# Optimization experiments

Hardware: AMD Instinct MI355X
Metric: run time of the kernel (lower is better)

## Reference

```python
import jax, jax.numpy as jnp
import numpy as np

CHANNELS = 512
NUM_HEADS = 8
GROUPS = 32
EPS = 1e-5  # torch GroupNorm default


def setup_inputs() -> dict:
    key = jax.random.key(0)
    ks = jax.random.split(key, 7)
    B, C, H, W = 16, CHANNELS, 64, 64
    x = jax.random.normal(ks[0], (B, C, H, W), dtype=jnp.float32)
    # GroupNorm affine params (torch init: weight=1, bias=0; randomize slightly for a nontrivial baseline)
    gamma = jnp.ones((C,), jnp.float32) + 0.02 * jax.random.normal(ks[1], (C,), jnp.float32)
    beta = 0.02 * jax.random.normal(ks[2], (C,), jnp.float32)
    # 1x1 convs == dense matrices over channel dim
    w_qkv = jax.random.normal(ks[3], (3 * C, C), jnp.float32) / np.sqrt(C)
    b_qkv = 0.01 * jax.random.normal(ks[4], (3 * C,), jnp.float32)
    w_proj = jax.random.normal(ks[5], (C, C), jnp.float32) / np.sqrt(C)
    b_proj = 0.01 * jax.random.normal(ks[6], (C,), jnp.float32)
    return {"x": x, "gamma": gamma, "beta": beta, "w_qkv": w_qkv,
            "b_qkv": b_qkv, "w_proj": w_proj, "b_proj": b_proj}


def _group_norm(x, gamma, beta):
    B, C, H, W = x.shape
    xg = x.reshape(B, GROUPS, C // GROUPS, H, W)
    mean = jnp.mean(xg, axis=(2, 3, 4), keepdims=True)
    var = jnp.mean(jnp.square(xg - mean), axis=(2, 3, 4), keepdims=True)
    xn = ((xg - mean) * jax.lax.rsqrt(var + EPS)).reshape(B, C, H, W)
    return xn * gamma[:, None, None] + beta[:, None, None]


def reference(x, gamma, beta, w_qkv, b_qkv, w_proj, b_proj):
    B, C, H, W = x.shape
    h = NUM_HEADS
    d = C // h  # head_dim
    residual = x
    xn = _group_norm(x, gamma, beta)
    # 1x1 conv == per-pixel dense layer over channels
    qkv = jnp.einsum('bchw,oc->bohw', xn, w_qkv) + b_qkv[:, None, None]
    q, k, v = jnp.split(qkv, 3, axis=1)
    N = H * W
    # rearrange 'b (h c) h1 w1 -> b h c (h1 w1)': rows = head_dim, cols = spatial
    q = q.reshape(B, h, d, N)
    k = k.reshape(B, h, d, N)
    v = v.reshape(B, h, d, N)
    scale = d ** (-0.5)
    # attention over head_dim axis (faithful to the source rearrange)
    attn = jax.nn.softmax(jnp.einsum('bhcn,bhdn->bhcd', q, k) * scale, axis=-1)  # [B,h,d,d]
    out = jnp.einsum('bhcd,bhdn->bhcn', attn, v).reshape(B, C, H, W)
    out = jnp.einsum('bchw,oc->bohw', out, w_proj) + b_proj[:, None, None]
    return out + residual
```

## Files before the change

kernel.cpp:

```cpp
#include <hip/hip_runtime.h>

typedef unsigned short u16;
typedef __attribute__((ext_vector_type(8))) short short8;
typedef __attribute__((ext_vector_type(4))) float floatx4;
typedef __attribute__((ext_vector_type(4))) unsigned int uintx4;

#define B_    16
#define C_    512
#define N_    4096
#define NH_   8
#define HD_   64
#define MQKV  1536

union V16 { uintx4 u; u16 s[8]; short8 h; };

__device__ inline u16 f2bf(float f) {
  union { float f; unsigned int i; } c; c.f = f;
  unsigned int i = c.i;
  return (u16)((i + 0x7FFFu + ((i >> 16) & 1u)) >> 16);
}

__device__ __forceinline__ void gld16(const u16* g, u16* l) {
  __builtin_amdgcn_global_load_lds(
      (const __attribute__((address_space(1))) unsigned int*)g,
      (__attribute__((address_space(3))) unsigned int*)l, 16, 0, 0);
}

__global__ __launch_bounds__(256) void gn_stats(const float* __restrict__ x,
    const float* __restrict__ gamma, const float* __restrict__ beta,
    float* __restrict__ s_arr, float* __restrict__ t_arr) {
  int b = blockIdx.x >> 5, g = blockIdx.x & 31;
  const floatx4* p = (const floatx4*)(x + (size_t)(b * C_ + g * 16) * N_);
  int tid = threadIdx.x;
  float sum = 0.f, ssq = 0.f;
  for (int it = 0; it < 64; ++it) {
    floatx4 v = p[tid + it * 256];
#pragma unroll
    for (int j = 0; j < 4; ++j) { float f = v[j]; sum += f; ssq += f * f; }
  }
#pragma unroll
  for (int off = 32; off > 0; off >>= 1) {
    sum += __shfl_down(sum, off);
    ssq += __shfl_down(ssq, off);
  }
  __shared__ float red[8];
  __shared__ float mv[2];
  int lane = tid & 63, wid = tid >> 6;
  if (lane == 0) { red[wid] = sum; red[wid + 4] = ssq; }
  __syncthreads();
  if (tid == 0) {
    float s = red[0] + red[1] + red[2] + red[3];
    float q = red[4] + red[5] + red[6] + red[7];
    float mean = s * (1.f / 65536.f);
    float var  = q * (1.f / 65536.f) - mean * mean;
    mv[0] = mean; mv[1] = rsqrtf(var + 1e-5f);
  }
  __syncthreads();
  if (tid < 16) {
    int c = g * 16 + tid;
    float ga = gamma[c], be = beta[c];
    float mean = mv[0], rstd = mv[1];
    s_arr[b * C_ + c] = ga * rstd;
    t_arr[b * C_ + c] = be - mean * rstd * ga;
  }
}

__global__ __launch_bounds__(256) void cvt_bf16(const float* __restrict__ src,
                                                u16* __restrict__ dst) {
  int i = blockIdx.x * 256 + threadIdx.x;
  const floatx4* s4 = (const floatx4*)src;
  floatx4 a = s4[2 * i], b = s4[2 * i + 1];
  V16 v;
#pragma unroll
  for (int j = 0; j < 4; ++j) { v.s[j] = f2bf(a[j]); v.s[4 + j] = f2bf(b[j]); }
  ((uintx4*)dst)[i] = v.u;
}

__global__ __launch_bounds__(256) void gn_apply_t(const float* __restrict__ x,
    const float* __restrict__ s_arr, const float* __restrict__ t_arr,
    u16* __restrict__ xt, int b0) {
  __shared__ float T[64][65];
  int bz = blockIdx.z, gb = b0 + bz;
  int n0 = blockIdx.x * 64, c0 = blockIdx.y * 64;
  int tid = threadIdx.x;
  int cl = tid >> 4;
  int nl = (tid & 15) * 4;
  const float* xb = x + (size_t)bz * C_ * N_;
#pragma unroll
  for (int ci = 0; ci < 4; ++ci) {
    int c = c0 + cl + ci * 16;
    float s = s_arr[gb * C_ + c], t = t_arr[gb * C_ + c];
    floatx4 v = *(const floatx4*)(xb + (size_t)c * N_ + n0 + nl);
#pragma unroll
    for (int j = 0; j < 4; ++j) T[cl + ci * 16][nl + j] = s * v[j] + t;
  }
  __syncthreads();
  int n = tid >> 2, cc = (tid & 3) * 16;
  V16 a, b;
#pragma unroll
  for (int j = 0; j < 8; ++j) a.s[j] = f2bf(T[cc + j][n]);
#pragma unroll
  for (int j = 0; j < 8; ++j) b.s[j] = f2bf(T[cc + 8 + j][n]);
  uintx4* dst = (uintx4*)(xt + (size_t)bz * N_ * C_ + (size_t)(n0 + n) * C_ + c0 + cc);
  dst[0] = a.u; dst[1] = b.u;
}

__global__ __launch_bounds__(256) void gemm_bt(
    const u16* __restrict__ A, const u16* __restrict__ Bm,
    const float* __restrict__ bias, const float* __restrict__ resid,
    void* __restrict__ outv, int M, int doRes, int outF32) {
  __shared__ alignas(16) u16 As[128 * 64];
  __shared__ alignas(16) u16 Bs[128 * 64];
  int bz = blockIdx.z;
  int m0 = blockIdx.y * 128, n0 = blockIdx.x * 128;
  int tid = threadIdx.x, lane = tid & 63, wid = tid >> 6;
  int quad = lane >> 4, l15 = lane & 15;
  int wm = (wid >> 1) * 64, wn = (wid & 1) * 64;
  int sr = tid >> 3, sc = tid & 7;
  const u16* Bb = Bm + (size_t)bz * ((size_t)N_ * C_);
  floatx4 acc[4][4];
#pragma unroll
  for (int i = 0; i < 4; ++i)
#pragma unroll
    for (int j = 0; j < 4; ++j) acc[i][j] = (floatx4)0.f;

  for (int kt = 0; kt < 8; ++kt) {
#pragma unroll
    for (int i = 0; i < 4; ++i) {
      int rr = sr + i * 32;
      int cc = sc ^ (rr & 7);
      gld16(A  + (size_t)(m0 + rr) * C_ + kt * 64 + cc * 8, &As[rr * 64 + sc * 8]);
      gld16(Bb + (size_t)(n0 + rr) * C_ + kt * 64 + cc * 8, &Bs[rr * 64 + sc * 8]);
    }
    __syncthreads();
#pragma unroll
    for (int ks = 0; ks < 2; ++ks) {
      short8 af[4], bf8[4];
#pragma unroll
      for (int mi = 0; mi < 4; ++mi) {
        int row = wm + mi * 16 + l15;
        int kc = (ks * 4 + quad) ^ (row & 7);
        af[mi] = *(const short8*)&As[row * 64 + kc * 8];
      }
#pragma unroll
      for (int ni = 0; ni < 4; ++ni) {
        int row = wn + ni * 16 + l15;
        int kc = (ks * 4 + quad) ^ (row & 7);
        bf8[ni] = *(const short8*)&Bs[row * 64 + kc * 8];
      }
#pragma unroll
      for (int mi = 0; mi < 4; ++mi)
#pragma unroll
        for (int ni = 0; ni < 4; ++ni)
          acc[mi][ni] = __builtin_amdgcn_mfma_f32_16x16x32_bf16(af[mi], bf8[ni], acc[mi][ni], 0, 0, 0);
    }
    __syncthreads();
  }
#pragma unroll
  for (int mi = 0; mi < 4; ++mi) {
#pragma unroll
    for (int ni = 0; ni < 4; ++ni) {
#pragma unroll
      for (int r = 0; r < 4; ++r) {
        int o = m0 + wm + mi * 16 + quad * 4 + r;
        int n = n0 + wn + ni * 16 + l15;
        float vv = acc[mi][ni][r] + bias[o];
        size_t oidx = ((size_t)bz * M + o) * N_ + n;
        if (doRes) vv += resid[oidx];
        if (outF32) ((float*)outv)[oidx] = vv;
        else        ((u16*)outv)[oidx]   = f2bf(vv);
      }
    }
  }
}

__global__ __launch_bounds__(256) void qk_softmax(const u16* __restrict__ qkv,
                                                  float* __restrict__ attn) {
  int h = blockIdx.x, bz = blockIdx.y;
  const u16* qb = qkv + ((size_t)bz * MQKV + h * HD_) * N_;
  const u16* kb = qkv + ((size_t)bz * MQKV + C_ + h * HD_) * N_;
  int tid = threadIdx.x, lane = tid & 63, wid = tid >> 6;
  int quad = lane >> 4, l15 = lane & 15;
  floatx4 acc[4][4];
#pragma unroll
  for (int i = 0; i < 4; ++i)
#pragma unroll
    for (int j = 0; j < 4; ++j) acc[i][j] = (floatx4)0.f;

  for (int ks = 0; ks < 32; ++ks) {
    int n = wid * 1024 + ks * 32 + quad * 8;
    short8 af[4], bf8[4];
#pragma unroll
    for (int mi = 0; mi < 4; ++mi)
      af[mi] = *(const short8*)(qb + (size_t)(mi * 16 + l15) * N_ + n);
#pragma unroll
    for (int ni = 0; ni < 4; ++ni)
      bf8[ni] = *(const short8*)(kb + (size_t)(ni * 16 + l15) * N_ + n);
#pragma unroll
    for (int mi = 0; mi < 4; ++mi)
#pragma unroll
      for (int ni = 0; ni < 4; ++ni)
        acc[mi][ni] = __builtin_amdgcn_mfma_f32_16x16x32_bf16(af[mi], bf8[ni], acc[mi][ni], 0, 0, 0);
  }
  __shared__ float S[64 * 65];
  for (int i = tid; i < 64 * 65; i += 256) S[i] = 0.f;
  __syncthreads();
#pragma unroll
  for (int mi = 0; mi < 4; ++mi)
#pragma unroll
    for (int ni = 0; ni < 4; ++ni)
#pragma unroll
      for (int r = 0; r < 4; ++r)
        atomicAdd(&S[(mi * 16 + quad * 4 + r) * 65 + ni * 16 + l15], acc[mi][ni][r]);
  __syncthreads();
  if (tid < 64) {
    float mx = -1e30f;
    for (int j = 0; j < 64; ++j) mx = fmaxf(mx, S[tid * 65 + j]);
    float sum = 0.f;
    for (int j = 0; j < 64; ++j) sum += __expf((S[tid * 65 + j] - mx) * 0.125f);
    float inv = 1.f / sum;
    float* dst = attn + ((size_t)(bz * NH_ + h) * 64 + tid) * 64;
    for (int j = 0; j < 64; ++j) dst[j] = __expf((S[tid * 65 + j] - mx) * 0.125f) * inv;
  }
}

__global__ __launch_bounds__(256) void pv_kernel(const float* __restrict__ attn,
    const u16* __restrict__ qkv, u16* __restrict__ ot) {
  int nt = blockIdx.x, h = blockIdx.y, bz = blockIdx.z;
  int n0 = nt * 256;
  const u16* vb = qkv + ((size_t)bz * MQKV + 2 * C_ + h * HD_) * N_;
  __shared__ alignas(16) u16 Ps[64 * 72];
  __shared__ alignas(16) u16 Vs[256 * 72];
  int tid = threadIdx.x, lane = tid & 63, wid = tid >> 6;
  int quad = lane >> 4, l15 = lane & 15;
  const float* ab = attn + (size_t)(bz * NH_ + h) * 4096;
#pragma unroll
  for (int i = 0; i < 16; ++i) {
    int idx = tid + i * 256;
    int row = idx >> 6, col = idx & 63;
    Ps[row * 72 + col] = f2bf(ab[idx]);
  }
#pragma unroll
  for (int i = 0; i < 8; ++i) {
    int l = tid + i * 256;
    int ch = l >> 5, n8 = (l & 31) * 8;
    V16 v; v.u = *(const uintx4*)(vb + (size_t)ch * N_ + n0 + n8);
    int chunk = ch >> 3, clo = ch & 7;
#pragma unroll
    for (int j = 0; j < 8; ++j) {
      int nl = n8 + j;
      Vs[nl * 72 + (chunk ^ ((nl >> 3) & 7)) * 8 + clo] = v.s[j];
    }
  }
  __syncthreads();
  floatx4 acc[4][4];
#pragma unroll
  for (int i = 0; i < 4; ++i)
#pragma unroll
    for (int j = 0; j < 4; ++j) acc[i][j] = (floatx4)0.f;
#pragma unroll
  for (int ks = 0; ks < 2; ++ks) {
    short8 af[4], bf8[4];
    int ko = ks * 32 + quad * 8;
#pragma unroll
    for (int mi = 0; mi < 4; ++mi)
      af[mi] = *(const short8*)&Ps[(mi * 16 + l15) * 72 + ko];
    int chunk = ks * 4 + quad;
#pragma unroll
    for (int ni = 0; ni < 4; ++ni) {
      int nl = wid * 64 + ni * 16 + l15;
      bf8[ni] = *(const short8*)&Vs[nl * 72 + (chunk ^ ((nl >> 3) & 7)) * 8];
    }
#pragma unroll
    for (int mi = 0; mi < 4; ++mi)
#pragma unroll
      for (int ni = 0; ni < 4; ++ni)
        acc[mi][ni] = __builtin_amdgcn_mfma_f32_16x16x32_bf16(af[mi], bf8[ni], acc[mi][ni], 0, 0, 0);
  }
  __syncthreads();
  u16* Ls = Vs;
#pragma unroll
  for (int mi = 0; mi < 4; ++mi)
#pragma unroll
    for (int ni = 0; ni < 4; ++ni)
#pragma unroll
      for (int r = 0; r < 4; ++r) {
        int n  = wid * 64 + ni * 16 + l15;
        int hd = mi * 16 + quad * 4 + r;
        Ls[n * 64 + (((hd >> 3) ^ (n & 7)) * 8) + (hd & 7)] = f2bf(acc[mi][ni][r]);
      }
  __syncthreads();
  uintx4* dst = (uintx4*)(ot + ((size_t)bz * N_ + n0 + tid) * C_ + h * HD_);
#pragma unroll
  for (int k = 0; k < 8; ++k) {
    int kc = k ^ (tid & 7);
    dst[k] = *(const uintx4*)&Ls[tid * 64 + kc * 8];
  }
}

extern "C" void kernel_launch(void* const* d_in, const int* in_sizes, int n_in,
                              void* d_out, int out_size, void* d_ws, size_t ws_size,
                              hipStream_t stream) {
  const float* x      = (const float*)d_in[0];
  const float* gamma  = (const float*)d_in[1];
  const float* beta   = (const float*)d_in[2];
  const float* w_qkv  = (const float*)d_in[3];
  const float* b_qkv  = (const float*)d_in[4];
  const float* w_proj = (const float*)d_in[5];
  const float* b_proj = (const float*)d_in[6];
  float* out = (float*)d_out;

  const size_t fixed = (size_t)2 * B_ * C_ * 4 + (size_t)(MQKV + C_) * C_ * 2;
  const size_t per_batch = (size_t)NH_ * 64 * 64 * 4 + (size_t)N_ * C_ * 2 + (size_t)MQKV * N_ * 2;
  int Bc = 16;
  while (Bc > 1 && fixed + (size_t)Bc * per_batch > ws_size) Bc >>= 1;

  float* s_arr = (float*)d_ws;
  float* t_arr = s_arr + B_ * C_;
  u16* wq = (u16*)(t_arr + B_ * C_);
  u16* wp = wq + MQKV * C_;
  float* attn = (float*)(wp + C_ * C_);
  u16* xt  = (u16*)(attn + (size_t)Bc * NH_ * 64 * 64);
  u16* qkv = xt + (size_t)Bc * N_ * C_;

  gn_stats<<<dim3(B_ * 32), dim3(256), 0, stream>>>(x, gamma, beta, s_arr, t_arr);
  cvt_bf16<<<dim3(MQKV * C_ / 2048), dim3(256), 0, stream>>>(w_qkv, wq);
  cvt_bf16<<<dim3(C_ * C_ / 2048), dim3(256), 0, stream>>>(w_proj, wp);

  for (int b0 = 0; b0 < B_; b0 += Bc) {
    gn_apply_t<<<dim3(N_ / 64, C_ / 64, Bc), dim3(256), 0, stream>>>(
        x + (size_t)b0 * C_ * N_, s_arr, t_arr, xt, b0);
    gemm_bt<<<dim3(32, 12, Bc), dim3(256), 0, stream>>>(
        wq, xt, b_qkv, nullptr, qkv, MQKV, 0, 0);
    qk_softmax<<<dim3(NH_, Bc), dim3(256), 0, stream>>>(qkv, attn);
    pv_kernel<<<dim3(16, NH_, Bc), dim3(256), 0, stream>>>(attn, qkv, xt);
    gemm_bt<<<dim3(32, 4, Bc), dim3(256), 0, stream>>>(
        wp, xt, b_proj, x + (size_t)b0 * C_ * N_, out + (size_t)b0 * C_ * N_, C_, 1, 1);
  }
}
```

Before: 787.1 us.

## Split QK reduction across spatial chunks and stage GEMM epilogue through LDS

The QK^T kernel, which used to launch only B*8 blocks, is split into 8 partial blocks per head over the spatial axis. Each block writes a 64x64 partial sum to a scratch area that reuses the xt buffer, and a new softmax_rows kernel adds the partials and applies the row softmax. This raises parallelism for the low-occupancy reduction at the cost of an extra launch and extra global traffic. The GEMM epilogue also now stages results in swizzled shared memory so the bf16 and fp32 outputs, including the residual add, are written with coalesced 16-byte vector stores instead of scattered scalar stores.

```diff
diff --git a/kernel.cpp b/kernel.cpp
--- a/kernel.cpp
+++ b/kernel.cpp
@@ -11,6 +11,7 @@
 #define NH_   8
 #define HD_   64
 #define MQKV  1536
+#define NSPL  8
 
 union V16 { uintx4 u; u16 s[8]; short8 h; };
 
@@ -109,8 +110,9 @@
     const u16* __restrict__ A, const u16* __restrict__ Bm,
     const float* __restrict__ bias, const float* __restrict__ resid,
     void* __restrict__ outv, int M, int doRes, int outF32) {
-  __shared__ alignas(16) u16 As[128 * 64];
-  __shared__ alignas(16) u16 Bs[128 * 64];
+  __shared__ alignas(16) u16 smem[128 * 64 * 2];
+  u16* As = smem;
+  u16* Bs = smem + 128 * 64;
   int bz = blockIdx.z;
   int m0 = blockIdx.y * 128, n0 = blockIdx.x * 128;
   int tid = threadIdx.x, lane = tid & 63, wid = tid >> 6;
@@ -156,27 +158,66 @@
     }
     __syncthreads();
   }
-#pragma unroll
-  for (int mi = 0; mi < 4; ++mi) {
-#pragma unroll
-    for (int ni = 0; ni < 4; ++ni) {
-#pragma unroll
-      for (int r = 0; r < 4; ++r) {
-        int o = m0 + wm + mi * 16 + quad * 4 + r;
-        int n = n0 + wn + ni * 16 + l15;
-        float vv = acc[mi][ni][r] + bias[o];
-        size_t oidx = ((size_t)bz * M + o) * N_ + n;
-        if (doRes) vv += resid[oidx];
-        if (outF32) ((float*)outv)[oidx] = vv;
-        else        ((u16*)outv)[oidx]   = f2bf(vv);
+  if (!outF32) {
+    u16* E = smem;
+#pragma unroll
+    for (int mi = 0; mi < 4; ++mi)
+#pragma unroll
+      for (int ni = 0; ni < 4; ++ni)
+#pragma unroll
+        for (int r = 0; r < 4; ++r) {
+          int row = wm + mi * 16 + quad * 4 + r;
+          int col = wn + ni * 16 + l15;
+          int ch = col >> 3;
+          int cs = (ch & 8) | ((ch & 7) ^ (row & 7));
+          E[row * 128 + cs * 8 + (col & 7)] = f2bf(acc[mi][ni][r] + bias[m0 + row]);
+        }
+    __syncthreads();
+    int row = tid >> 1, half = tid & 1;
+    u16* orow = (u16*)outv + ((size_t)bz * M + m0 + row) * N_ + n0 + half * 64;
+#pragma unroll
+    for (int k = 0; k < 8; ++k) {
+      int cs = (half * 8) | (k ^ (row & 7));
+      *(uintx4*)(orow + k * 8) = *(const uintx4*)&E[row * 128 + cs * 8];
+    }
+  } else {
+    float* E = (float*)smem;
+#pragma unroll
+    for (int p = 0; p < 2; ++p) {
+#pragma unroll
+      for (int q = 0; q < 2; ++q)
+#pragma unroll
+        for (int ni = 0; ni < 4; ++ni)
+#pragma unroll
+          for (int r = 0; r < 4; ++r) {
+            int mi = p * 2 + q;
+            int lr = (wid >> 1) * 32 + q * 16 + quad * 4 + r;
+            int col = wn + ni * 16 + l15;
+            int ch = col >> 2;
+            int cs = (ch & ~7) | ((ch & 7) ^ (lr & 7));
+            E[lr * 128 + cs * 4 + (col & 3)] =
+                acc[mi][ni][r] + bias[m0 + wm + mi * 16 + quad * 4 + r];
+          }
+      __syncthreads();
+      int lr = tid >> 2, qt = tid & 3;
+      int o = m0 + (lr >> 5) * 64 + p * 32 + (lr & 31);
+      size_t obase = ((size_t)bz * M + o) * N_ + n0 + qt * 4;
+#pragma unroll
+      for (int k = 0; k < 8; ++k) {
+        int ch = k * 4 + qt;
+        int cs = (ch & ~7) | ((ch & 7) ^ (lr & 7));
+        floatx4 v = *(const floatx4*)&E[lr * 128 + cs * 4];
+        if (doRes) v += *(const floatx4*)(resid + obase + (size_t)k * 16);
+        *(floatx4*)((float*)outv + obase + (size_t)k * 16) = v;
       }
-    }
-  }
-}
-
-__global__ __launch_bounds__(256) void qk_softmax(const u16* __restrict__ qkv,
-                                                  float* __restrict__ attn) {
-  int h = blockIdx.x, bz = blockIdx.y;
+      if (p == 0) __syncthreads();
+    }
+  }
+}
+
+__global__ __launch_bounds__(256) void qk_partial(const u16* __restrict__ qkv,
+    float* __restrict__ spart, int nbh) {
+  int h = blockIdx.x, bz = blockIdx.y, p = blockIdx.z;
   const u16* qb = qkv + ((size_t)bz * MQKV + h * HD_) * N_;
   const u16* kb = qkv + ((size_t)bz * MQKV + C_ + h * HD_) * N_;
   int tid = threadIdx.x, lane = tid & 63, wid = tid >> 6;
@@ -187,8 +228,8 @@
 #pragma unroll
     for (int j = 0; j < 4; ++j) acc[i][j] = (floatx4)0.f;
 
-  for (int ks = 0; ks < 32; ++ks) {
-    int n = wid * 1024 + ks * 32 + quad * 8;
+  for (int ks = 0; ks < 4; ++ks) {
+    int n = p * 512 + wid * 128 + ks * 32 + quad * 8;
     short8 af[4], bf8[4];
 #pragma unroll
     for (int mi = 0; mi < 4; ++mi)
@@ -202,8 +243,8 @@
       for (int ni = 0; ni < 4; ++ni)
         acc[mi][ni] = __builtin_amdgcn_mfma_f32_16x16x32_bf16(af[mi], bf8[ni], acc[mi][ni], 0, 0, 0);
   }
-  __shared__ float S[64 * 65];
-  for (int i = tid; i < 64 * 65; i += 256) S[i] = 0.f;
+  __shared__ float S[64 * 68];
+  for (int i = tid; i < 64 * 68; i += 256) S[i] = 0.f;
   __syncthreads();
 #pragma unroll
   for (int mi = 0; mi < 4; ++mi)
@@ -211,17 +252,46 @@
     for (int ni = 0; ni < 4; ++ni)
 #pragma unroll
       for (int r = 0; r < 4; ++r)
-        atomicAdd(&S[(mi * 16 + quad * 4 + r) * 65 + ni * 16 + l15], acc[mi][ni][r]);
-  __syncthreads();
-  if (tid < 64) {
-    float mx = -1e30f;
-    for (int j = 0; j < 64; ++j) mx = fmaxf(mx, S[tid * 65 + j]);
-    float sum = 0.f;
-    for (int j = 0; j < 64; ++j) sum += __expf((S[tid * 65 + j] - mx) * 0.125f);
-    float inv = 1.f / sum;
-    float* dst = attn + ((size_t)(bz * NH_ + h) * 64 + tid) * 64;
-    for (int j = 0; j < 64; ++j) dst[j] = __expf((S[tid * 65 + j] - mx) * 0.125f) * inv;
-  }
+        atomicAdd(&S[(mi * 16 + quad * 4 + r) * 68 + ni * 16 + l15], acc[mi][ni][r]);
+  __syncthreads();
+  int bh = bz * NH_ + h;
+  float* dst = spart + ((size_t)p * nbh + bh) * 4096 + tid * 16;
+  int row = tid >> 2, c0 = (tid & 3) * 16;
+#pragma unroll
+  for (int j = 0; j < 4; ++j)
+    *(floatx4*)(dst + j * 4) = *(const floatx4*)&S[row * 68 + c0 + j * 4];
+}
+
+__global__ __launch_bounds__(64) void softmax_rows(const float* __restrict__ spart,
+    float* __restrict__ attn, int nbh) {
+  int bh = blockIdx.x, c = threadIdx.x;
+  const float* sp = spart + (size_t)bh * 4096 + c * 64;
+  floatx4 row4[16];
+#pragma unroll
+  for (int j = 0; j < 16; ++j) row4[j] = *(const floatx4*)(sp + j * 4);
+#pragma unroll
+  for (int p = 1; p < NSPL; ++p) {
+    const float* spp = sp + (size_t)p * nbh * 4096;
+#pragma unroll
+    for (int j = 0; j < 16; ++j) row4[j] += *(const floatx4*)(spp + j * 4);
+  }
+  float mx = -1e30f;
+#pragma unroll
+  for (int j = 0; j < 16; ++j)
+#pragma unroll
+    for (int e = 0; e < 4; ++e) mx = fmaxf(mx, row4[j][e]);
+  float sum = 0.f;
+#pragma unroll
+  for (int j = 0; j < 16; ++j)
+#pragma unroll
+    for (int e = 0; e < 4; ++e) {
+      float ev = __expf((row4[j][e] - mx) * 0.125f);
+      row4[j][e] = ev; sum += ev;
+    }
+  float inv = 1.f / sum;
+  float* dst = attn + (size_t)bh * 4096 + c * 64;
+#pragma unroll
+  for (int j = 0; j < 16; ++j) *(floatx4*)(dst + j * 4) = row4[j] * inv;
 }
 
 __global__ __launch_bounds__(256) void pv_kernel(const float* __restrict__ attn,
@@ -322,17 +392,20 @@
   float* attn = (float*)(wp + C_ * C_);
   u16* xt  = (u16*)(attn + (size_t)Bc * NH_ * 64 * 64);
   u16* qkv = xt + (size_t)Bc * N_ * C_;
+  float* spart = (float*)xt;
 
   gn_stats<<<dim3(B_ * 32), dim3(256), 0, stream>>>(x, gamma, beta, s_arr, t_arr);
   cvt_bf16<<<dim3(MQKV * C_ / 2048), dim3(256), 0, stream>>>(w_qkv, wq);
   cvt_bf16<<<dim3(C_ * C_ / 2048), dim3(256), 0, stream>>>(w_proj, wp);
 
   for (int b0 = 0; b0 < B_; b0 += Bc) {
+    int nbh = Bc * NH_;
     gn_apply_t<<<dim3(N_ / 64, C_ / 64, Bc), dim3(256), 0, stream>>>(
         x + (size_t)b0 * C_ * N_, s_arr, t_arr, xt, b0);
     gemm_bt<<<dim3(32, 12, Bc), dim3(256), 0, stream>>>(
         wq, xt, b_qkv, nullptr, qkv, MQKV, 0, 0);
-    qk_softmax<<<dim3(NH_, Bc), dim3(256), 0, stream>>>(qkv, attn);
+    qk_partial<<<dim3(NH_, Bc, NSPL), dim3(256), 0, stream>>>(qkv, spart, nbh);
+    softmax_rows<<<dim3(nbh), dim3(64), 0, stream>>>(spart, attn, nbh);
     pv_kernel<<<dim3(16, NH_, Bc), dim3(256), 0, stream>>>(attn, qkv, xt);
     gemm_bt<<<dim3(32, 4, Bc), dim3(256), 0, stream>>>(
         wp, xt, b_proj, x + (size_t)b0 * C_ * N_, out + (size_t)b0 * C_ * N_, C_, 1, 1);
```

Result: faster. 698.2 us (-11.3%).
